# Optimization experiments

Measured on AMD Instinct MI355X. Metric: run time of the kernel, lower is better.

Reference implementation:

```python
import jax, jax.numpy as jnp
import numpy as np
import math

B, S, F_IN = 8, 1024, 32
D, H, L, NCLS = 512, 8, 6, 3
DFF = 4 * D
DK = D // H
EPS = 1e-5


def make_pe(max_len, d_model):
    pos = jnp.arange(max_len, dtype=jnp.float32)[:, None]
    div = jnp.exp(jnp.arange(0, d_model, 2, dtype=jnp.float32) * (-math.log(10000.0) / d_model))
    pe = jnp.zeros((max_len, d_model), dtype=jnp.float32)
    pe = pe.at[:, 0::2].set(jnp.sin(pos * div))
    pe = pe.at[:, 1::2].set(jnp.cos(pos * div))
    return pe  # [max_len, D]


def layernorm(x, g, b):
    m = jnp.mean(x, -1, keepdims=True)
    v = jnp.mean((x - m) ** 2, -1, keepdims=True)
    return (x - m) * jax.lax.rsqrt(v + EPS) * g + b


def setup_inputs() -> dict:
    key = jax.random.key(0)
    ks = iter(jax.random.split(key, 40))

    def w(shape, scale=None):
        k = next(ks)
        s = scale if scale is not None else 1.0 / math.sqrt(shape[0])
        return jax.random.normal(k, shape, dtype=jnp.float32) * s

    inp = {
        'x': jax.random.normal(next(ks), (B, S, F_IN), dtype=jnp.float32),
        'pe': make_pe(S, D),
        'emb_w': w((F_IN, D)), 'emb_b': jnp.zeros((D,), jnp.float32),
        'Wq': w((L, D, D)), 'bq': jnp.zeros((L, D), jnp.float32),
        'Wk': w((L, D, D)), 'bk': jnp.zeros((L, D), jnp.float32),
        'Wv': w((L, D, D)), 'bv': jnp.zeros((L, D), jnp.float32),
        'Wo': w((L, D, D)), 'bo': jnp.zeros((L, D), jnp.float32),
        'ln1_g': jnp.ones((L, D), jnp.float32), 'ln1_b': jnp.zeros((L, D), jnp.float32),
        'ln2_g': jnp.ones((L, D), jnp.float32), 'ln2_b': jnp.zeros((L, D), jnp.float32),
        'W1': w((L, D, DFF)), 'b1': jnp.zeros((L, DFF), jnp.float32),
        'W2': w((L, DFF, D)), 'b2': jnp.zeros((L, D), jnp.float32),
        'fc1_w': w((D, 256)), 'fc1_b': jnp.zeros((256,), jnp.float32),
        'fc2_w': w((256, 128)), 'fc2_b': jnp.zeros((128,), jnp.float32),
        'fc3_w': w((128, NCLS)), 'fc3_b': jnp.zeros((NCLS,), jnp.float32),
    }
    return inp


def reference(x, pe, emb_w, emb_b, Wq, bq, Wk, bk, Wv, bv, Wo, bo,
              ln1_g, ln1_b, ln2_g, ln2_b, W1, b1, W2, b2,
              fc1_w, fc1_b, fc2_w, fc2_b, fc3_w, fc3_b):
    scale = math.sqrt(DK)
    h = x @ emb_w + emb_b                      # [B,S,D]
    h = h + pe[None, :S, :]                    # positional encoding
    for l in range(L):
        # multi-head self-attention (full O(S^2) scores, as in source)
        q = (h @ Wq[l] + bq[l]).reshape(B, S, H, DK).transpose(0, 2, 1, 3)
        k = (h @ Wk[l] + bk[l]).reshape(B, S, H, DK).transpose(0, 2, 1, 3)
        v = (h @ Wv[l] + bv[l]).reshape(B, S, H, DK).transpose(0, 2, 1, 3)
        scores = jnp.einsum('bhqd,bhkd->bhqk', q, k) / scale   # [B,H,S,S]
        attn = jax.nn.softmax(scores, axis=-1)
        ctx = jnp.einsum('bhqk,bhkd->bhqd', attn, v)           # [B,H,S,DK]
        ctx = ctx.transpose(0, 2, 1, 3).reshape(B, S, D)
        attn_out = ctx @ Wo[l] + bo[l]
        h = layernorm(h + attn_out, ln1_g[l], ln1_b[l])
        ff = jax.nn.relu(h @ W1[l] + b1[l]) @ W2[l] + b2[l]
        h = layernorm(h + ff, ln2_g[l], ln2_b[l])
    pooled = jnp.mean(h, axis=1)               # AdaptiveAvgPool1d(1) over seq
    z = jax.nn.relu(pooled @ fc1_w + fc1_b)
    z = jax.nn.relu(z @ fc2_w + fc2_b)
    return z @ fc3_w + fc3_b                   # [B, NCLS]
```

## Files before the change

### kernel.cpp

```cpp
#include <hip/hip_runtime.h>
#include <math.h>

#define B_   8
#define S_   1024
#define FIN  32
#define D_   512
#define H_   8
#define L_   6
#define DFF_ 2048
#define DK_  64

__device__ __forceinline__ float mulrn(float a, float b) { return __fmul_rn(a, b); }
__device__ __forceinline__ float addrn(float a, float b) { return __fadd_rn(a, b); }

__global__ __launch_bounds__(128) void k_embed(const float* __restrict__ x,
                                               const float* __restrict__ emb_w,
                                               const float* __restrict__ emb_b,
                                               const float* __restrict__ pe,
                                               float* __restrict__ h) {
    int row = blockIdx.x;
    int s = row & (S_ - 1);
    int t = threadIdx.x;
    __shared__ float xs[FIN];
    if (t < FIN) xs[t] = x[row * FIN + t];
    __syncthreads();
    int d = t * 4;
    float a0 = 0.f, a1 = 0.f, a2 = 0.f, a3 = 0.f;
#pragma unroll
    for (int k = 0; k < FIN; ++k) {
        float xv = xs[k];
        const float* wr = &emb_w[k * D_ + d];
        a0 = fmaf(xv, wr[0], a0);
        a1 = fmaf(xv, wr[1], a1);
        a2 = fmaf(xv, wr[2], a2);
        a3 = fmaf(xv, wr[3], a3);
    }
    const float* bb = &emb_b[d];
    const float* pp = &pe[s * D_ + d];
    float4 o;
    o.x = addrn(addrn(a0, bb[0]), pp[0]);
    o.y = addrn(addrn(a1, bb[1]), pp[1]);
    o.z = addrn(addrn(a2, bb[2]), pp[2]);
    o.w = addrn(addrn(a3, bb[3]), pp[3]);
    *(float4*)&h[(size_t)row * D_ + d] = o;
}

template<bool RELU>
__global__ __launch_bounds__(256) void k_gemm(const float* __restrict__ A,
                                              const float* __restrict__ W,
                                              const float* __restrict__ bias,
                                              float* __restrict__ C,
                                              int M, int N, int K) {
    __shared__ float As[2][16][68];
    __shared__ float Bs[2][16][68];
    int bm = blockIdx.y * 64, bn = blockIdx.x * 64;
    int t = threadIdx.x;
    int tr = t >> 4, tc = t & 15;
    int ar = t >> 2, ak = (t & 3) * 4;
    int wk = t >> 4, wn = (t & 15) * 4;
    float acc[4][4] = {};

    float4 pa = *(const float4*)&A[(size_t)(bm + ar) * K + ak];
    float4 pw = *(const float4*)&W[(size_t)wk * N + bn + wn];
    As[0][ak + 0][ar] = pa.x; As[0][ak + 1][ar] = pa.y;
    As[0][ak + 2][ar] = pa.z; As[0][ak + 3][ar] = pa.w;
    *(float4*)&Bs[0][wk][wn] = pw;
    __syncthreads();

    const int nP = K >> 4;
    for (int p = 0; p < nP; ++p) {
        int cur = p & 1;
        if (p + 1 < nP) {
            pa = *(const float4*)&A[(size_t)(bm + ar) * K + (p + 1) * 16 + ak];
            pw = *(const float4*)&W[(size_t)((p + 1) * 16 + wk) * N + bn + wn];
        }
#pragma unroll
        for (int kk = 0; kk < 16; ++kk) {
            float4 av = *(const float4*)&As[cur][kk][tr * 4];
            float4 bv = *(const float4*)&Bs[cur][kk][tc * 4];
            acc[0][0] = fmaf(av.x, bv.x, acc[0][0]); acc[0][1] = fmaf(av.x, bv.y, acc[0][1]);
            acc[0][2] = fmaf(av.x, bv.z, acc[0][2]); acc[0][3] = fmaf(av.x, bv.w, acc[0][3]);
            acc[1][0] = fmaf(av.y, bv.x, acc[1][0]); acc[1][1] = fmaf(av.y, bv.y, acc[1][1]);
            acc[1][2] = fmaf(av.y, bv.z, acc[1][2]); acc[1][3] = fmaf(av.y, bv.w, acc[1][3]);
            acc[2][0] = fmaf(av.z, bv.x, acc[2][0]); acc[2][1] = fmaf(av.z, bv.y, acc[2][1]);
            acc[2][2] = fmaf(av.z, bv.z, acc[2][2]); acc[2][3] = fmaf(av.z, bv.w, acc[2][3]);
            acc[3][0] = fmaf(av.w, bv.x, acc[3][0]); acc[3][1] = fmaf(av.w, bv.y, acc[3][1]);
            acc[3][2] = fmaf(av.w, bv.z, acc[3][2]); acc[3][3] = fmaf(av.w, bv.w, acc[3][3]);
        }
        if (p + 1 < nP) {
            int nxt = cur ^ 1;
            As[nxt][ak + 0][ar] = pa.x; As[nxt][ak + 1][ar] = pa.y;
            As[nxt][ak + 2][ar] = pa.z; As[nxt][ak + 3][ar] = pa.w;
            *(float4*)&Bs[nxt][wk][wn] = pw;
        }
        __syncthreads();
    }
    float4 b4 = *(const float4*)&bias[bn + tc * 4];
#pragma unroll
    for (int i = 0; i < 4; ++i) {
        float4 o;
        o.x = addrn(acc[i][0], b4.x); o.y = addrn(acc[i][1], b4.y);
        o.z = addrn(acc[i][2], b4.z); o.w = addrn(acc[i][3], b4.w);
        if (RELU) {
            o.x = fmaxf(o.x, 0.f); o.y = fmaxf(o.y, 0.f);
            o.z = fmaxf(o.z, 0.f); o.w = fmaxf(o.w, 0.f);
        }
        *(float4*)&C[(size_t)(bm + tr * 4 + i) * N + bn + tc * 4] = o;
    }
}

__global__ __launch_bounds__(256) void k_attn(const float* q,
                                              const float* __restrict__ kg,
                                              const float* __restrict__ vg,
                                              float* ctx) {
    __shared__ float KVs[32][68];
    __shared__ float Ss[16 * 1024];
    int hh = blockIdx.x;
    int ch = blockIdx.y;
    int b  = blockIdx.z;
    int t  = threadIdx.x;
    int r  = t >> 4, c16 = t & 15;
    const int row0 = ch * 16;
    const size_t base = (size_t)b * S_ * D_ + hh * DK_;
    const int srr = t >> 4, scc = (t & 15) * 4;

    *(float4*)&KVs[srr][scc] = *(const float4*)&q[base + (size_t)(row0 + srr) * D_ + scc];
    __syncthreads();
    float4 qr[16];
#pragma unroll
    for (int i = 0; i < 16; ++i) qr[i] = *(float4*)&KVs[r][i * 4];

    float4 nx0 = *(const float4*)&kg[base + (size_t)srr * D_ + scc];
    float4 nx1 = *(const float4*)&kg[base + (size_t)(srr + 16) * D_ + scc];
    __syncthreads();
    *(float4*)&KVs[srr][scc] = nx0;
    *(float4*)&KVs[srr + 16][scc] = nx1;
    __syncthreads();
    for (int kt = 0; kt < 32; ++kt) {
        if (kt < 31) {
            size_t rowb = base + (size_t)((kt + 1) * 32) * D_;
            nx0 = *(const float4*)&kg[rowb + (size_t)srr * D_ + scc];
            nx1 = *(const float4*)&kg[rowb + (size_t)(srr + 16) * D_ + scc];
        }
        float s0 = 0.f, s1 = 0.f;
#pragma unroll
        for (int d4 = 0; d4 < 16; ++d4) {
            float4 qv = qr[d4];
            float4 k0 = *(float4*)&KVs[c16][d4 * 4];
            float4 k1 = *(float4*)&KVs[c16 + 16][d4 * 4];
            s0 = addrn(s0, mulrn(qv.x, k0.x)); s1 = addrn(s1, mulrn(qv.x, k1.x));
            s0 = addrn(s0, mulrn(qv.y, k0.y)); s1 = addrn(s1, mulrn(qv.y, k1.y));
            s0 = addrn(s0, mulrn(qv.z, k0.z)); s1 = addrn(s1, mulrn(qv.z, k1.z));
            s0 = addrn(s0, mulrn(qv.w, k0.w)); s1 = addrn(s1, mulrn(qv.w, k1.w));
        }
#pragma unroll
        for (int u = 0; u < 2; ++u) {
            int jglob = kt * 32 + u * 16 + c16;
            int sl = jglob >> 6, jj = jglob & 63;
            Ss[(r << 10) + (sl << 6) + ((jj + sl + (r << 3)) & 63)] =
                mulrn(u == 0 ? s0 : s1, 0.125f);
        }
        __syncthreads();
        if (kt < 31) {
            *(float4*)&KVs[srr][scc] = nx0;
            *(float4*)&KVs[srr + 16][scc] = nx1;
            __syncthreads();
        }
    }

    const int sbase = (r << 10) + (c16 << 6);
    const int rot   = (c16 + (r << 3)) & 63;
    float mx = -INFINITY;
    {
        int off = rot;
        for (int j = 0; j < 64; ++j) {
            mx = fmaxf(mx, Ss[sbase + off]);
            off = (off + 1) & 63;
        }
    }
    mx = fmaxf(mx, __shfl_xor(mx, 1));
    mx = fmaxf(mx, __shfl_xor(mx, 2));
    mx = fmaxf(mx, __shfl_xor(mx, 4));
    mx = fmaxf(mx, __shfl_xor(mx, 8));

    float psum = 0.f;
    {
        int off = rot;
        for (int j = 0; j < 64; ++j) {
            int p_ = sbase + off;
            float p = expf(__fsub_rn(Ss[p_], mx));
            Ss[p_] = p;
            psum = addrn(psum, p);
            off = (off + 1) & 63;
        }
    }
    psum = addrn(psum, __shfl_xor(psum, 1));
    psum = addrn(psum, __shfl_xor(psum, 2));
    psum = addrn(psum, __shfl_xor(psum, 4));
    psum = addrn(psum, __shfl_xor(psum, 8));
    {
        int off = rot;
        for (int j = 0; j < 64; ++j) {
            int p_ = sbase + off;
            Ss[p_] = __fdiv_rn(Ss[p_], psum);
            off = (off + 1) & 63;
        }
    }

    int d0 = c16 * 4;
    float a0 = 0.f, a1 = 0.f, a2 = 0.f, a3 = 0.f;
    nx0 = *(const float4*)&vg[base + (size_t)srr * D_ + scc];
    nx1 = *(const float4*)&vg[base + (size_t)(srr + 16) * D_ + scc];
    __syncthreads();
    *(float4*)&KVs[srr][scc] = nx0;
    *(float4*)&KVs[srr + 16][scc] = nx1;
    __syncthreads();
    for (int vt = 0; vt < 32; ++vt) {
        if (vt < 31) {
            size_t rowb = base + (size_t)((vt + 1) * 32) * D_;
            nx0 = *(const float4*)&vg[rowb + (size_t)srr * D_ + scc];
            nx1 = *(const float4*)&vg[rowb + (size_t)(srr + 16) * D_ + scc];
        }
        int sl = vt >> 1;
        const float* srow = &Ss[(r << 10) + (sl << 6)];
        int off = (((vt & 1) << 5) + sl + (r << 3)) & 63;
#pragma unroll 8
        for (int jl = 0; jl < 32; ++jl) {
            float p = srow[off];
            off = (off + 1) & 63;
            float4 v4 = *(float4*)&KVs[jl][d0];
            a0 = addrn(a0, mulrn(p, v4.x));
            a1 = addrn(a1, mulrn(p, v4.y));
            a2 = addrn(a2, mulrn(p, v4.z));
            a3 = addrn(a3, mulrn(p, v4.w));
        }
        __syncthreads();
        if (vt < 31) {
            *(float4*)&KVs[srr][scc] = nx0;
            *(float4*)&KVs[srr + 16][scc] = nx1;
            __syncthreads();
        }
    }
    float4 o = {a0, a1, a2, a3};
    *(float4*)&ctx[base + (size_t)(row0 + r) * D_ + d0] = o;
}

__global__ __launch_bounds__(256) void k_add_ln(float* h,
                                                const float* __restrict__ res,
                                                const float* __restrict__ g,
                                                const float* __restrict__ bta) {
    int row = blockIdx.x;
    int t = threadIdx.x;
    size_t base = (size_t)row * D_;
    float y0 = addrn(h[base + t],       res[base + t]);
    float y1 = addrn(h[base + t + 256], res[base + t + 256]);
    __shared__ float red[4];
    int w = t >> 6;
    float s = y0 + y1;
#pragma unroll
    for (int o = 1; o < 64; o <<= 1) s += __shfl_xor(s, o);
    if ((t & 63) == 0) red[w] = s;
    __syncthreads();
    float mean = (red[0] + red[1] + red[2] + red[3]) * (1.f / D_);
    __syncthreads();
    float d0 = __fsub_rn(y0, mean), d1 = __fsub_rn(y1, mean);
    s = mulrn(d0, d0) + mulrn(d1, d1);
#pragma unroll
    for (int o = 1; o < 64; o <<= 1) s += __shfl_xor(s, o);
    if ((t & 63) == 0) red[w] = s;
    __syncthreads();
    float var = (red[0] + red[1] + red[2] + red[3]) * (1.f / D_);
    float rstd = __fdiv_rn(1.0f, sqrtf(__fadd_rn(var, 1e-5f)));
    h[base + t]       = addrn(mulrn(mulrn(d0, rstd), g[t]),       bta[t]);
    h[base + t + 256] = addrn(mulrn(mulrn(d1, rstd), g[t + 256]), bta[t + 256]);
}

__global__ __launch_bounds__(256) void k_pool(const float* __restrict__ h,
                                              float* __restrict__ pooled) {
    int blk = blockIdx.x;
    int b = blk >> 3, dc = (blk & 7) * 64;
    int t = threadIdx.x;
    int d = dc + (t & 63), sg = t >> 6;
    float s = 0.f;
    for (int ss = sg; ss < S_; ss += 4)
        s = addrn(s, h[((size_t)b * S_ + ss) * D_ + d]);
    __shared__ float sh[4][64];
    sh[sg][t & 63] = s;
    __syncthreads();
    if (t < 64)
        pooled[b * D_ + dc + t] = (sh[0][t] + sh[1][t] + sh[2][t] + sh[3][t]) * (1.f / S_);
}

__global__ __launch_bounds__(256) void k_head(const float* __restrict__ pooled,
                                              const float* __restrict__ w1, const float* __restrict__ b1,
                                              const float* __restrict__ w2, const float* __restrict__ b2,
                                              const float* __restrict__ w3, const float* __restrict__ b3,
                                              float* __restrict__ out) {
    __shared__ float ps[B_][D_];
    __shared__ float z1[B_][256];
    __shared__ float z2[B_][128];
    int t = threadIdx.x;
    for (int i = t; i < B_ * D_; i += 256) ps[i >> 9][i & 511] = pooled[i];
    __syncthreads();
    {
        float acc[B_] = {};
        for (int k = 0; k < D_; ++k) {
            float w = w1[k * 256 + t];
#pragma unroll
            for (int b = 0; b < B_; ++b) acc[b] = fmaf(ps[b][k], w, acc[b]);
        }
#pragma unroll
        for (int b = 0; b < B_; ++b) z1[b][t] = fmaxf(addrn(acc[b], b1[t]), 0.f);
    }
    __syncthreads();
    if (t < 128) {
        float acc[B_] = {};
        for (int k = 0; k < 256; ++k) {
            float w = w2[k * 128 + t];
#pragma unroll
            for (int b = 0; b < B_; ++b) acc[b] = fmaf(z1[b][k], w, acc[b]);
        }
#pragma unroll
        for (int b = 0; b < B_; ++b) z2[b][t] = fmaxf(addrn(acc[b], b2[t]), 0.f);
    }
    __syncthreads();
    if (t < B_ * 3) {
        int b = t / 3, c = t % 3;
        float acc = 0.f;
        for (int k = 0; k < 128; ++k) acc = fmaf(z2[b][k], w3[k * 3 + c], acc);
        out[t] = addrn(acc, b3[c]);
    }
}

extern "C" void kernel_launch(void* const* d_in, const int* in_sizes, int n_in,
                              void* d_out, int out_size, void* d_ws, size_t ws_size,
                              hipStream_t stream) {
    const float* x     = (const float*)d_in[0];
    const float* pe    = (const float*)d_in[1];
    const float* emb_w = (const float*)d_in[2];
    const float* emb_b = (const float*)d_in[3];
    const float* Wq    = (const float*)d_in[4];
    const float* bq    = (const float*)d_in[5];
    const float* Wk    = (const float*)d_in[6];
    const float* bk    = (const float*)d_in[7];
    const float* Wv    = (const float*)d_in[8];
    const float* bv    = (const float*)d_in[9];
    const float* Wo    = (const float*)d_in[10];
    const float* bo    = (const float*)d_in[11];
    const float* ln1_g = (const float*)d_in[12];
    const float* ln1_b = (const float*)d_in[13];
    const float* ln2_g = (const float*)d_in[14];
    const float* ln2_b = (const float*)d_in[15];
    const float* W1    = (const float*)d_in[16];
    const float* b1    = (const float*)d_in[17];
    const float* W2    = (const float*)d_in[18];
    const float* b2    = (const float*)d_in[19];
    const float* fc1_w = (const float*)d_in[20];
    const float* fc1_b = (const float*)d_in[21];
    const float* fc2_w = (const float*)d_in[22];
    const float* fc2_b = (const float*)d_in[23];
    const float* fc3_w = (const float*)d_in[24];
    const float* fc3_b = (const float*)d_in[25];

    const size_t NBS = (size_t)B_ * S_ * D_;
    float* ws = (float*)d_ws;
    const int MROWS = B_ * S_;

    float* h = ws;
    float* q = h + NBS;
    float* k = q + NBS;
    float* v = k + NBS;
    float* pooled = v + NBS;

    k_embed<<<MROWS, 128, 0, stream>>>(x, emb_w, emb_b, pe, h);

    dim3 g512(D_ / 64, MROWS / 64);
    dim3 gff(DFF_ / 64, 4096 / 64);
    dim3 gw2(D_ / 64, 4096 / 64);
    dim3 gattn(H_, S_ / 16, B_);

    for (int l = 0; l < L_; ++l) {
        const float* wq = Wq + (size_t)l * D_ * D_;
        const float* wk = Wk + (size_t)l * D_ * D_;
        const float* wv = Wv + (size_t)l * D_ * D_;
        const float* wo = Wo + (size_t)l * D_ * D_;
        k_gemm<false><<<g512, 256, 0, stream>>>(h, wq, bq + l * D_, q, MROWS, D_, D_);
        k_gemm<false><<<g512, 256, 0, stream>>>(h, wk, bk + l * D_, k, MROWS, D_, D_);
        k_gemm<false><<<g512, 256, 0, stream>>>(h, wv, bv + l * D_, v, MROWS, D_, D_);
        k_attn<<<gattn, 256, 0, stream>>>(q, k, v, q);
        k_gemm<false><<<g512, 256, 0, stream>>>(q, wo, bo + l * D_, k, MROWS, D_, D_);
        k_add_ln<<<MROWS, 256, 0, stream>>>(h, k, ln1_g + l * D_, ln1_b + l * D_);
        for (int c = 0; c < 2; ++c) {
            float* ff1 = q;
            k_gemm<true ><<<gff, 256, 0, stream>>>(h + (size_t)c * 4096 * D_,
                W1 + (size_t)l * D_ * DFF_, b1 + l * DFF_, ff1, 4096, DFF_, D_);
            k_gemm<false><<<gw2, 256, 0, stream>>>(ff1,
                W2 + (size_t)l * DFF_ * D_, b2 + l * D_, v + (size_t)c * 4096 * D_, 4096, D_, DFF_);
        }
        k_add_ln<<<MROWS, 256, 0, stream>>>(h, v, ln2_g + l * D_, ln2_b + l * D_);
    }

    k_pool<<<B_ * 8, 256, 0, stream>>>(h, pooled);
    k_head<<<1, 256, 0, stream>>>(pooled, fc1_w, fc1_b, fc2_w, fc2_b, fc3_w, fc3_b, (float*)d_out);
}
```

Before: 7.914 ms.

## Widen GEMM tile to 64x128 and restructure attention score shared layout

The GEMM block tile grows from 64x64 to 64x128, so each thread computes a 4x8 output micro-tile and each loaded A element is reused across twice as many columns. The launch grids are halved to match. Separately, the attention score buffer is reorganized into a padded [64][16][17] layout, which replaces the rotating-offset indexing and lets the softmax and PV loops unroll fully. The cost is more accumulator registers per thread and fewer GEMM blocks, which may lower occupancy.

```diff
diff --git a/kernel.cpp b/kernel.cpp
--- a/kernel.cpp
+++ b/kernel.cpp
@@ -52,60 +52,79 @@
                                               float* __restrict__ C,
                                               int M, int N, int K) {
     __shared__ float As[2][16][68];
-    __shared__ float Bs[2][16][68];
-    int bm = blockIdx.y * 64, bn = blockIdx.x * 64;
+    __shared__ float Bs[2][16][132];
+    int bm = blockIdx.y * 64, bn = blockIdx.x * 128;
     int t = threadIdx.x;
     int tr = t >> 4, tc = t & 15;
     int ar = t >> 2, ak = (t & 3) * 4;
-    int wk = t >> 4, wn = (t & 15) * 4;
-    float acc[4][4] = {};
-
-    float4 pa = *(const float4*)&A[(size_t)(bm + ar) * K + ak];
-    float4 pw = *(const float4*)&W[(size_t)wk * N + bn + wn];
+    int wk = t >> 5, wn = (t & 31) * 4;
+    float acc[4][8] = {};
+
+    float4 pa  = *(const float4*)&A[(size_t)(bm + ar) * K + ak];
+    float4 pw0 = *(const float4*)&W[(size_t)wk * N + bn + wn];
+    float4 pw1 = *(const float4*)&W[(size_t)(wk + 8) * N + bn + wn];
     As[0][ak + 0][ar] = pa.x; As[0][ak + 1][ar] = pa.y;
     As[0][ak + 2][ar] = pa.z; As[0][ak + 3][ar] = pa.w;
-    *(float4*)&Bs[0][wk][wn] = pw;
+    *(float4*)&Bs[0][wk][wn]     = pw0;
+    *(float4*)&Bs[0][wk + 8][wn] = pw1;
     __syncthreads();
 
     const int nP = K >> 4;
     for (int p = 0; p < nP; ++p) {
         int cur = p & 1;
         if (p + 1 < nP) {
-            pa = *(const float4*)&A[(size_t)(bm + ar) * K + (p + 1) * 16 + ak];
-            pw = *(const float4*)&W[(size_t)((p + 1) * 16 + wk) * N + bn + wn];
+            pa  = *(const float4*)&A[(size_t)(bm + ar) * K + (p + 1) * 16 + ak];
+            pw0 = *(const float4*)&W[(size_t)((p + 1) * 16 + wk) * N + bn + wn];
+            pw1 = *(const float4*)&W[(size_t)((p + 1) * 16 + wk + 8) * N + bn + wn];
         }
 #pragma unroll
         for (int kk = 0; kk < 16; ++kk) {
             float4 av = *(const float4*)&As[cur][kk][tr * 4];
-            float4 bv = *(const float4*)&Bs[cur][kk][tc * 4];
-            acc[0][0] = fmaf(av.x, bv.x, acc[0][0]); acc[0][1] = fmaf(av.x, bv.y, acc[0][1]);
-            acc[0][2] = fmaf(av.x, bv.z, acc[0][2]); acc[0][3] = fmaf(av.x, bv.w, acc[0][3]);
-            acc[1][0] = fmaf(av.y, bv.x, acc[1][0]); acc[1][1] = fmaf(av.y, bv.y, acc[1][1]);
-            acc[1][2] = fmaf(av.y, bv.z, acc[1][2]); acc[1][3] = fmaf(av.y, bv.w, acc[1][3]);
-            acc[2][0] = fmaf(av.z, bv.x, acc[2][0]); acc[2][1] = fmaf(av.z, bv.y, acc[2][1]);
-            acc[2][2] = fmaf(av.z, bv.z, acc[2][2]); acc[2][3] = fmaf(av.z, bv.w, acc[2][3]);
-            acc[3][0] = fmaf(av.w, bv.x, acc[3][0]); acc[3][1] = fmaf(av.w, bv.y, acc[3][1]);
-            acc[3][2] = fmaf(av.w, bv.z, acc[3][2]); acc[3][3] = fmaf(av.w, bv.w, acc[3][3]);
+            float4 b0 = *(const float4*)&Bs[cur][kk][tc * 8];
+            float4 b1 = *(const float4*)&Bs[cur][kk][tc * 8 + 4];
+            acc[0][0] = fmaf(av.x, b0.x, acc[0][0]); acc[0][1] = fmaf(av.x, b0.y, acc[0][1]);
+            acc[0][2] = fmaf(av.x, b0.z, acc[0][2]); acc[0][3] = fmaf(av.x, b0.w, acc[0][3]);
+            acc[0][4] = fmaf(av.x, b1.x, acc[0][4]); acc[0][5] = fmaf(av.x, b1.y, acc[0][5]);
+            acc[0][6] = fmaf(av.x, b1.z, acc[0][6]); acc[0][7] = fmaf(av.x, b1.w, acc[0][7]);
+            acc[1][0] = fmaf(av.y, b0.x, acc[1][0]); acc[1][1] = fmaf(av.y, b0.y, acc[1][1]);
+            acc[1][2] = fmaf(av.y, b0.z, acc[1][2]); acc[1][3] = fmaf(av.y, b0.w, acc[1][3]);
+            acc[1][4] = fmaf(av.y, b1.x, acc[1][4]); acc[1][5] = fmaf(av.y, b1.y, acc[1][5]);
+            acc[1][6] = fmaf(av.y, b1.z, acc[1][6]); acc[1][7] = fmaf(av.y, b1.w, acc[1][7]);
+            acc[2][0] = fmaf(av.z, b0.x, acc[2][0]); acc[2][1] = fmaf(av.z, b0.y, acc[2][1]);
+            acc[2][2] = fmaf(av.z, b0.z, acc[2][2]); acc[2][3] = fmaf(av.z, b0.w, acc[2][3]);
+            acc[2][4] = fmaf(av.z, b1.x, acc[2][4]); acc[2][5] = fmaf(av.z, b1.y, acc[2][5]);
+            acc[2][6] = fmaf(av.z, b1.z, acc[2][6]); acc[2][7] = fmaf(av.z, b1.w, acc[2][7]);
+            acc[3][0] = fmaf(av.w, b0.x, acc[3][0]); acc[3][1] = fmaf(av.w, b0.y, acc[3][1]);
+            acc[3][2] = fmaf(av.w, b0.z, acc[3][2]); acc[3][3] = fmaf(av.w, b0.w, acc[3][3]);
+            acc[3][4] = fmaf(av.w, b1.x, acc[3][4]); acc[3][5] = fmaf(av.w, b1.y, acc[3][5]);
+            acc[3][6] = fmaf(av.w, b1.z, acc[3][6]); acc[3][7] = fmaf(av.w, b1.w, acc[3][7]);
         }
         if (p + 1 < nP) {
             int nxt = cur ^ 1;
             As[nxt][ak + 0][ar] = pa.x; As[nxt][ak + 1][ar] = pa.y;
             As[nxt][ak + 2][ar] = pa.z; As[nxt][ak + 3][ar] = pa.w;
-            *(float4*)&Bs[nxt][wk][wn] = pw;
+            *(float4*)&Bs[nxt][wk][wn]     = pw0;
+            *(float4*)&Bs[nxt][wk + 8][wn] = pw1;
         }
         __syncthreads();
     }
-    float4 b4 = *(const float4*)&bias[bn + tc * 4];
+    float4 ba = *(const float4*)&bias[bn + tc * 8];
+    float4 bb = *(const float4*)&bias[bn + tc * 8 + 4];
 #pragma unroll
     for (int i = 0; i < 4; ++i) {
-        float4 o;
-        o.x = addrn(acc[i][0], b4.x); o.y = addrn(acc[i][1], b4.y);
-        o.z = addrn(acc[i][2], b4.z); o.w = addrn(acc[i][3], b4.w);
+        float4 o0, o1;
+        o0.x = addrn(acc[i][0], ba.x); o0.y = addrn(acc[i][1], ba.y);
+        o0.z = addrn(acc[i][2], ba.z); o0.w = addrn(acc[i][3], ba.w);
+        o1.x = addrn(acc[i][4], bb.x); o1.y = addrn(acc[i][5], bb.y);
+        o1.z = addrn(acc[i][6], bb.z); o1.w = addrn(acc[i][7], bb.w);
         if (RELU) {
-            o.x = fmaxf(o.x, 0.f); o.y = fmaxf(o.y, 0.f);
-            o.z = fmaxf(o.z, 0.f); o.w = fmaxf(o.w, 0.f);
-        }
-        *(float4*)&C[(size_t)(bm + tr * 4 + i) * N + bn + tc * 4] = o;
+            o0.x = fmaxf(o0.x, 0.f); o0.y = fmaxf(o0.y, 0.f);
+            o0.z = fmaxf(o0.z, 0.f); o0.w = fmaxf(o0.w, 0.f);
+            o1.x = fmaxf(o1.x, 0.f); o1.y = fmaxf(o1.y, 0.f);
+            o1.z = fmaxf(o1.z, 0.f); o1.w = fmaxf(o1.w, 0.f);
+        }
+        *(float4*)&C[(size_t)(bm + tr * 4 + i) * N + bn + tc * 8]     = o0;
+        *(float4*)&C[(size_t)(bm + tr * 4 + i) * N + bn + tc * 8 + 4] = o1;
     }
 }
 
@@ -114,7 +133,7 @@
                                               const float* __restrict__ vg,
                                               float* ctx) {
     __shared__ float KVs[32][68];
-    __shared__ float Ss[16 * 1024];
+    __shared__ float Ss[64][16][17];
     int hh = blockIdx.x;
     int ch = blockIdx.y;
     int b  = blockIdx.z;
@@ -153,13 +172,10 @@
             s0 = addrn(s0, mulrn(qv.z, k0.z)); s1 = addrn(s1, mulrn(qv.z, k1.z));
             s0 = addrn(s0, mulrn(qv.w, k0.w)); s1 = addrn(s1, mulrn(qv.w, k1.w));
         }
-#pragma unroll
-        for (int u = 0; u < 2; ++u) {
-            int jglob = kt * 32 + u * 16 + c16;
-            int sl = jglob >> 6, jj = jglob & 63;
-            Ss[(r << 10) + (sl << 6) + ((jj + sl + (r << 3)) & 63)] =
-                mulrn(u == 0 ? s0 : s1, 0.125f);
-        }
+        int jg0 = kt * 32 + c16;
+        int jg1 = jg0 + 16;
+        Ss[jg0 & 63][jg0 >> 6][r] = mulrn(s0, 0.125f);
+        Ss[jg1 & 63][jg1 >> 6][r] = mulrn(s1, 0.125f);
         __syncthreads();
         if (kt < 31) {
             *(float4*)&KVs[srr][scc] = nx0;
@@ -168,44 +184,29 @@
         }
     }
 
-    const int sbase = (r << 10) + (c16 << 6);
-    const int rot   = (c16 + (r << 3)) & 63;
     float mx = -INFINITY;
-    {
-        int off = rot;
-        for (int j = 0; j < 64; ++j) {
-            mx = fmaxf(mx, Ss[sbase + off]);
-            off = (off + 1) & 63;
-        }
-    }
+#pragma unroll
+    for (int jj = 0; jj < 64; ++jj)
+        mx = fmaxf(mx, Ss[jj][c16][r]);
     mx = fmaxf(mx, __shfl_xor(mx, 1));
     mx = fmaxf(mx, __shfl_xor(mx, 2));
     mx = fmaxf(mx, __shfl_xor(mx, 4));
     mx = fmaxf(mx, __shfl_xor(mx, 8));
 
     float psum = 0.f;
-    {
-        int off = rot;
-        for (int j = 0; j < 64; ++j) {
-            int p_ = sbase + off;
-            float p = expf(__fsub_rn(Ss[p_], mx));
-            Ss[p_] = p;
-            psum = addrn(psum, p);
-            off = (off + 1) & 63;
-        }
+#pragma unroll
+    for (int jj = 0; jj < 64; ++jj) {
+        float p = expf(__fsub_rn(Ss[jj][c16][r], mx));
+        Ss[jj][c16][r] = p;
+        psum = addrn(psum, p);
     }
     psum = addrn(psum, __shfl_xor(psum, 1));
     psum = addrn(psum, __shfl_xor(psum, 2));
     psum = addrn(psum, __shfl_xor(psum, 4));
     psum = addrn(psum, __shfl_xor(psum, 8));
-    {
-        int off = rot;
-        for (int j = 0; j < 64; ++j) {
-            int p_ = sbase + off;
-            Ss[p_] = __fdiv_rn(Ss[p_], psum);
-            off = (off + 1) & 63;
-        }
-    }
+#pragma unroll
+    for (int jj = 0; jj < 64; ++jj)
+        Ss[jj][c16][r] = __fdiv_rn(Ss[jj][c16][r], psum);
 
     int d0 = c16 * 4;
     float a0 = 0.f, a1 = 0.f, a2 = 0.f, a3 = 0.f;
@@ -221,13 +222,10 @@
             nx0 = *(const float4*)&vg[rowb + (size_t)srr * D_ + scc];
             nx1 = *(const float4*)&vg[rowb + (size_t)(srr + 16) * D_ + scc];
         }
-        int sl = vt >> 1;
-        const float* srow = &Ss[(r << 10) + (sl << 6)];
-        int off = (((vt & 1) << 5) + sl + (r << 3)) & 63;
-#pragma unroll 8
+        const float* srow = &Ss[(vt & 1) * 32][vt >> 1][r];
+#pragma unroll
         for (int jl = 0; jl < 32; ++jl) {
-            float p = srow[off];
-            off = (off + 1) & 63;
+            float p = srow[jl * 272];
             float4 v4 = *(float4*)&KVs[jl][d0];
             a0 = addrn(a0, mulrn(p, v4.x));
             a1 = addrn(a1, mulrn(p, v4.y));
@@ -374,9 +372,9 @@
 
     k_embed<<<MROWS, 128, 0, stream>>>(x, emb_w, emb_b, pe, h);
 
-    dim3 g512(D_ / 64, MROWS / 64);
-    dim3 gff(DFF_ / 64, 4096 / 64);
-    dim3 gw2(D_ / 64, 4096 / 64);
+    dim3 g512(D_ / 128, MROWS / 64);
+    dim3 gff(DFF_ / 128, 4096 / 64);
+    dim3 gw2(D_ / 128, 4096 / 64);
     dim3 gattn(H_, S_ / 16, B_);
 
     for (int l = 0; l < L_; ++l) {
```

New measurement: 9.250 ms. +16.9%, slower.
